# Kernel optimization log

Measured on AMD Instinct MI355X. Metric: run time of the kernel, lower is better.

The kernel has to match this reference:

```python
import math
import jax, jax.numpy as jnp
import numpy as np

N, T, F, H = 30000, 4, 128, 8  # num_node, num_type, num_fea, num_head
D = F // H


def setup_inputs() -> dict:
    key = jax.random.key(0)
    k0, k1, k2, k3, k4 = jax.random.split(key, 5)
    feature = jax.random.normal(k0, (N, F), dtype=jnp.float32)
    edge_fea = jax.random.normal(k1, (N, T, F), dtype=jnp.float32)
    node_multi_mask = jax.random.randint(k2, (N,), 0, T)
    # Xavier-uniform-like scale for [*, F, F] projection tables
    xav = math.sqrt(6.0 / (F + F))
    node_proj = jax.random.uniform(k3, (T, F, F), minval=-xav, maxval=xav, dtype=jnp.float32)
    edge_proj = jax.random.uniform(k4, (T * T, F, F), minval=-xav, maxval=xav, dtype=jnp.float32)
    return {
        "feature": feature,
        "edge_fea": edge_fea,
        "node_multi_mask": node_multi_mask,
        "node_proj": node_proj,
        "edge_proj": edge_proj,
    }


def reference(feature, edge_fea, node_multi_mask, node_proj, edge_proj):
    # Type-indexed projections. Instead of gathering per-node [F,F] matrices
    # (which would materialize N*F*F), compute projections for all T source
    # types in one batched einsum, then select each node's type with a gather.
    # node: out[n] = node_proj[mask[n]] @ feature[n]
    node_all = jnp.einsum('tgf,nf->ntg', node_proj, feature)           # [N,T,F]
    node_p = jnp.take_along_axis(node_all, node_multi_mask[:, None, None], axis=1)[:, 0]  # [N,F]
    # edge: out[n,j] = edge_proj[mask[n]*T + j] @ edge_fea[n,j]
    edge_proj_r = edge_proj.reshape(T, T, F, F)                         # [src_type, j, F, F]
    edge_all = jnp.einsum('stgf,ntf->nstg', edge_proj_r, edge_fea)      # [N,T_src,T,F]
    edge_p = jnp.take_along_axis(edge_all, node_multi_mask[:, None, None, None], axis=1)[:, 0]  # [N,T,F]

    # multi-head attention weights
    node_multi_in = node_p.reshape(N, 1, H, D).transpose(0, 2, 1, 3) / math.sqrt(D)  # [N,H,1,D]
    edge_multi_in = edge_p.reshape(N, T, H, D).transpose(0, 2, 3, 1)                  # [N,H,D,T]
    scores = jnp.matmul(node_multi_in, edge_multi_in)                                 # [N,H,1,T]
    # NOTE: original uses nn.Softmax(dim=1) -> softmax over the HEAD axis
    all_r_weight = jax.nn.softmax(scores, axis=1).transpose(0, 3, 1, 2)               # [N,T,H,1]
    return all_r_weight
```

## Files before the change

### kernel.cpp

```cpp
#include <hip/hip_runtime.h>
#include <hip/hip_bf16.h>

#define N_NODES 30000
#define T_TYPES 4
#define F_DIM   128
#define H_HEADS 8

typedef __bf16 bf16x8 __attribute__((ext_vector_type(8)));
typedef __bf16 bf16x4 __attribute__((ext_vector_type(4)));
typedef float  floatx4 __attribute__((ext_vector_type(4)));

#define WS_REORDER 64
#define WS_NPB     480256
#define WS_EPB     611328

template <int CTRL>
static __device__ __forceinline__ float dpp_add(float x) {
    int xi = __builtin_bit_cast(int, x);
    int yi = __builtin_amdgcn_update_dpp(xi, xi, CTRL, 0xF, 0xF, true);
    return x + __builtin_bit_cast(float, yi);
}
static __device__ __forceinline__ float sum16(float x) {
    x = dpp_add<0xB1>(x);
    x = dpp_add<0x4E>(x);
    x = dpp_add<0x141>(x);
    x = dpp_add<0x140>(x);
    return x;
}

__global__ __launch_bounds__(256) void prep_bucket_kernel(
    const float* __restrict__ node_proj, const float* __restrict__ edge_proj,
    const int* __restrict__ mask,
    __bf16* __restrict__ npb, __bf16* __restrict__ epb,
    int* __restrict__ counts, int* __restrict__ reorder)
{
    if (blockIdx.x < 320) {
        int i = blockIdx.x * 256 + threadIdx.x;
        int base = i * 4;
        float4 v;
        __bf16* dst;
        if (base < T_TYPES * F_DIM * F_DIM) {
            v = ((const float4*)node_proj)[i];
            dst = npb + base;
        } else {
            int off = base - T_TYPES * F_DIM * F_DIM;
            v = ((const float4*)edge_proj)[off >> 2];
            dst = epb + off;
        }
        bf16x4 w = { (__bf16)v.x, (__bf16)v.y, (__bf16)v.z, (__bf16)v.w };
        *(bf16x4*)dst = w;
    } else {
        int n = (blockIdx.x - 320) * 256 + threadIdx.x;
        int lane = threadIdx.x & 63;
        int t = (n < N_NODES) ? mask[n] : -1;
        #pragma unroll
        for (int tt = 0; tt < T_TYPES; ++tt) {
            unsigned long long bm = __ballot(t == tt);
            if (bm == 0ull) continue;
            int cnt = __popcll(bm);
            int leader = __ffsll(bm) - 1;
            int base = 0;
            if (lane == leader) base = atomicAdd(&counts[tt], cnt);
            base = __shfl(base, leader);
            if (t == tt) {
                int prefix = __popcll(bm & ((1ull << lane) - 1ull));
                reorder[tt * N_NODES + base + prefix] = n;
            }
        }
    }
}

__global__ __launch_bounds__(256, 7) void main_kernel(
    const float* __restrict__ feature, const float* __restrict__ edge_fea,
    const int* __restrict__ counts, const int* __restrict__ reorder,
    const __bf16* __restrict__ npb, const __bf16* __restrict__ epb,
    float* __restrict__ out)
{
    const int b = blockIdx.x;
    const int t = b & 3;
    const int start = (b >> 2) * 32;
    const int Nt = counts[t];
    if (start >= Nt) return;
    const int valid = min(32, Nt - start);

    __shared__ __bf16 Afeat[32][136];
    __shared__ __bf16 Aedge[32][136];
    __shared__ float  sc[32][4][H_HEADS];
    __shared__ int    nidx[32];

    const int tid = threadIdx.x;
    if (tid < 32) {
        int s = (tid < valid) ? tid : (valid - 1);
        nidx[tid] = reorder[t * N_NODES + start + s];
    }
    __syncthreads();

    const int colv = tid & 31;
    const int rowg = tid >> 5;
    #pragma unroll
    for (int it = 0; it < 4; ++it) {
        int row = it * 8 + rowg;
        float4 v = ((const float4*)(feature + (long)nidx[row] * F_DIM))[colv];
        bf16x4 w = { (__bf16)v.x, (__bf16)v.y, (__bf16)v.z, (__bf16)v.w };
        *(bf16x4*)(&Afeat[row][0] + colv * 4) = w;
    }
    __syncthreads();

    const int lane = tid & 63;
    const int wave = tid >> 6;
    const int ml   = lane & 15;
    const int quad = lane >> 4;
    const int g0   = wave * 32;

    floatx4 accN[2][2] = {};
    {
        const __bf16* a0 = &Afeat[ml][quad * 8];
        const __bf16* a1 = &Afeat[16 + ml][quad * 8];
        const __bf16* b0 = npb + t * (F_DIM * F_DIM) + (g0 + ml) * F_DIM + quad * 8;
        const __bf16* b1 = b0 + 16 * F_DIM;
        #pragma unroll
        for (int k0 = 0; k0 < 128; k0 += 32) {
            bf16x8 A0 = *(const bf16x8*)(a0 + k0);
            bf16x8 A1 = *(const bf16x8*)(a1 + k0);
            bf16x8 B0 = *(const bf16x8*)(b0 + k0);
            bf16x8 B1 = *(const bf16x8*)(b1 + k0);
            accN[0][0] = __builtin_amdgcn_mfma_f32_16x16x32_bf16(A0, B0, accN[0][0], 0, 0, 0);
            accN[0][1] = __builtin_amdgcn_mfma_f32_16x16x32_bf16(A0, B1, accN[0][1], 0, 0, 0);
            accN[1][0] = __builtin_amdgcn_mfma_f32_16x16x32_bf16(A1, B0, accN[1][0], 0, 0, 0);
            accN[1][1] = __builtin_amdgcn_mfma_f32_16x16x32_bf16(A1, B1, accN[1][1], 0, 0, 0);
        }
    }

    #pragma unroll
    for (int j = 0; j < 4; ++j) {
        if (j > 0) __syncthreads();
        #pragma unroll
        for (int it = 0; it < 4; ++it) {
            int row = it * 8 + rowg;
            float4 v = ((const float4*)(edge_fea + ((long)nidx[row] * 4 + j) * F_DIM))[colv];
            bf16x4 w = { (__bf16)v.x, (__bf16)v.y, (__bf16)v.z, (__bf16)v.w };
            *(bf16x4*)(&Aedge[row][0] + colv * 4) = w;
        }
        __syncthreads();

        floatx4 accE[2][2] = {};
        {
            const __bf16* a0 = &Aedge[ml][quad * 8];
            const __bf16* a1 = &Aedge[16 + ml][quad * 8];
            const __bf16* b0 = epb + (t * 4 + j) * (F_DIM * F_DIM) + (g0 + ml) * F_DIM + quad * 8;
            const __bf16* b1 = b0 + 16 * F_DIM;
            #pragma unroll
            for (int k0 = 0; k0 < 128; k0 += 32) {
                bf16x8 A0 = *(const bf16x8*)(a0 + k0);
                bf16x8 A1 = *(const bf16x8*)(a1 + k0);
                bf16x8 B0 = *(const bf16x8*)(b0 + k0);
                bf16x8 B1 = *(const bf16x8*)(b1 + k0);
                accE[0][0] = __builtin_amdgcn_mfma_f32_16x16x32_bf16(A0, B0, accE[0][0], 0, 0, 0);
                accE[0][1] = __builtin_amdgcn_mfma_f32_16x16x32_bf16(A0, B1, accE[0][1], 0, 0, 0);
                accE[1][0] = __builtin_amdgcn_mfma_f32_16x16x32_bf16(A1, B0, accE[1][0], 0, 0, 0);
                accE[1][1] = __builtin_amdgcn_mfma_f32_16x16x32_bf16(A1, B1, accE[1][1], 0, 0, 0);
            }
        }
        #pragma unroll
        for (int mt = 0; mt < 2; ++mt) {
            #pragma unroll
            for (int nt = 0; nt < 2; ++nt) {
                floatx4 p = accN[mt][nt] * accE[mt][nt];
                p.x = sum16(p.x);
                p.y = sum16(p.y);
                p.z = sum16(p.z);
                p.w = sum16(p.w);
                if (ml == 0) {
                    int h = wave * 2 + nt;
                    int mb = mt * 16 + quad * 4;
                    sc[mb + 0][j][h] = p.x * 0.25f;
                    sc[mb + 1][j][h] = p.y * 0.25f;
                    sc[mb + 2][j][h] = p.z * 0.25f;
                    sc[mb + 3][j][h] = p.w * 0.25f;
                }
            }
        }
    }
    __syncthreads();

    if (tid < 128) {
        int node = tid >> 2, j = tid & 3;
        if (node < valid) {
            float v[8], m = -1e30f;
            #pragma unroll
            for (int h = 0; h < 8; ++h) { v[h] = sc[node][j][h]; m = fmaxf(m, v[h]); }
            float s = 0.f;
            #pragma unroll
            for (int h = 0; h < 8; ++h) { v[h] = __expf(v[h] - m); s += v[h]; }
            float r = 1.0f / s;
            float* o = out + (long)nidx[node] * (T_TYPES * H_HEADS) + j * H_HEADS;
            float4 o0 = { v[0] * r, v[1] * r, v[2] * r, v[3] * r };
            float4 o1 = { v[4] * r, v[5] * r, v[6] * r, v[7] * r };
            ((float4*)o)[0] = o0;
            ((float4*)o)[1] = o1;
        }
    }
}

extern "C" void kernel_launch(void* const* d_in, const int* in_sizes, int n_in,
                              void* d_out, int out_size, void* d_ws, size_t ws_size,
                              hipStream_t stream) {
    const float* feature   = (const float*)d_in[0];
    const float* edge_fea  = (const float*)d_in[1];
    const int*   mask      = (const int*)d_in[2];
    const float* node_proj = (const float*)d_in[3];
    const float* edge_proj = (const float*)d_in[4];
    float* out = (float*)d_out;

    char* ws = (char*)d_ws;
    int*    counts  = (int*)ws;
    int*    reorder = (int*)(ws + WS_REORDER);
    __bf16* npb     = (__bf16*)(ws + WS_NPB);
    __bf16* epb     = (__bf16*)(ws + WS_EPB);

    hipMemsetAsync(counts, 0, 4 * sizeof(int), stream);
    prep_bucket_kernel<<<320 + (N_NODES + 255) / 256, 256, 0, stream>>>(
        node_proj, edge_proj, mask, npb, epb, counts, reorder);
    int nblk = ((N_NODES + 31) / 32) * T_TYPES;
    main_kernel<<<nblk, 256, 0, stream>>>(feature, edge_fea, counts, reorder, npb, epb, out);
}
```

Before: 146.2 us.

## Replace global type bucketing with per-block local type grouping

Drops the global atomic bucketing pass, the memset and the reorder buffer. Each block now handles 32 consecutive nodes and groups them by type locally with ballots in shared memory. All four edge rows are loaded in one pass, which removes the per-j barriers, and output writes become contiguous. In exchange, a block runs up to four partially filled 16-row MFMA tiles, one per type present, so MFMA work can roughly double. Occupancy is also lowered to 3 waves per SIMD because the shared edge buffer is larger.

```diff
diff --git a/kernel.cpp b/kernel.cpp
--- a/kernel.cpp
+++ b/kernel.cpp
@@ -5,14 +5,13 @@
 #define T_TYPES 4
 #define F_DIM   128
 #define H_HEADS 8
+#define NBLK    ((N_NODES + 31) / 32)
 
 typedef __bf16 bf16x8 __attribute__((ext_vector_type(8)));
 typedef __bf16 bf16x4 __attribute__((ext_vector_type(4)));
 typedef float  floatx4 __attribute__((ext_vector_type(4)));
 
-#define WS_REORDER 64
-#define WS_NPB     480256
-#define WS_EPB     611328
+#define WS_EPB 131072
 
 template <int CTRL>
 static __device__ __forceinline__ float dpp_add(float x) {
@@ -28,81 +27,78 @@
     return x;
 }
 
-__global__ __launch_bounds__(256) void prep_bucket_kernel(
+__global__ __launch_bounds__(256) void prep_kernel(
     const float* __restrict__ node_proj, const float* __restrict__ edge_proj,
+    __bf16* __restrict__ npb, __bf16* __restrict__ epb)
+{
+    int i = blockIdx.x * 256 + threadIdx.x;
+    int base = i * 4;
+    float4 v;
+    __bf16* dst;
+    if (base < T_TYPES * F_DIM * F_DIM) {
+        v = ((const float4*)node_proj)[i];
+        dst = npb + base;
+    } else {
+        int off = base - T_TYPES * F_DIM * F_DIM;
+        v = ((const float4*)edge_proj)[off >> 2];
+        dst = epb + off;
+    }
+    bf16x4 w = { (__bf16)v.x, (__bf16)v.y, (__bf16)v.z, (__bf16)v.w };
+    *(bf16x4*)dst = w;
+}
+
+__global__ __launch_bounds__(256, 3) void main_kernel(
+    const float* __restrict__ feature, const float* __restrict__ edge_fea,
     const int* __restrict__ mask,
-    __bf16* __restrict__ npb, __bf16* __restrict__ epb,
-    int* __restrict__ counts, int* __restrict__ reorder)
+    const __bf16* __restrict__ npb, const __bf16* __restrict__ epb,
+    float* __restrict__ out)
 {
-    if (blockIdx.x < 320) {
-        int i = blockIdx.x * 256 + threadIdx.x;
-        int base = i * 4;
-        float4 v;
-        __bf16* dst;
-        if (base < T_TYPES * F_DIM * F_DIM) {
-            v = ((const float4*)node_proj)[i];
-            dst = npb + base;
-        } else {
-            int off = base - T_TYPES * F_DIM * F_DIM;
-            v = ((const float4*)edge_proj)[off >> 2];
-            dst = epb + off;
-        }
-        bf16x4 w = { (__bf16)v.x, (__bf16)v.y, (__bf16)v.z, (__bf16)v.w };
-        *(bf16x4*)dst = w;
-    } else {
-        int n = (blockIdx.x - 320) * 256 + threadIdx.x;
-        int lane = threadIdx.x & 63;
-        int t = (n < N_NODES) ? mask[n] : -1;
+    const int n0 = blockIdx.x * 32;
+    const int valid = min(32, N_NODES - n0);
+
+    __shared__ __bf16 Afeat[32][136];
+    __shared__ __bf16 Aedge[4][32][136];
+    __shared__ float  sc[32][4][H_HEADS];
+    __shared__ int    perm[32];
+    __shared__ int    goff[T_TYPES], gcnt[T_TYPES];
+
+    const int tid = threadIdx.x;
+
+    if (tid < 64) {
+        int lane = tid;
+        int t = (lane < valid) ? mask[n0 + lane] : -1;
+        int base = 0;
         #pragma unroll
         for (int tt = 0; tt < T_TYPES; ++tt) {
             unsigned long long bm = __ballot(t == tt);
-            if (bm == 0ull) continue;
             int cnt = __popcll(bm);
-            int leader = __ffsll(bm) - 1;
-            int base = 0;
-            if (lane == leader) base = atomicAdd(&counts[tt], cnt);
-            base = __shfl(base, leader);
+            if (lane == 0) { goff[tt] = base; gcnt[tt] = cnt; }
             if (t == tt) {
-                int prefix = __popcll(bm & ((1ull << lane) - 1ull));
-                reorder[tt * N_NODES + base + prefix] = n;
+                int slot = base + __popcll(bm & ((1ull << lane) - 1ull));
+                perm[slot] = lane;
             }
+            base += cnt;
         }
     }
-}
-
-__global__ __launch_bounds__(256, 7) void main_kernel(
-    const float* __restrict__ feature, const float* __restrict__ edge_fea,
-    const int* __restrict__ counts, const int* __restrict__ reorder,
-    const __bf16* __restrict__ npb, const __bf16* __restrict__ epb,
-    float* __restrict__ out)
-{
-    const int b = blockIdx.x;
-    const int t = b & 3;
-    const int start = (b >> 2) * 32;
-    const int Nt = counts[t];
-    if (start >= Nt) return;
-    const int valid = min(32, Nt - start);
-
-    __shared__ __bf16 Afeat[32][136];
-    __shared__ __bf16 Aedge[32][136];
-    __shared__ float  sc[32][4][H_HEADS];
-    __shared__ int    nidx[32];
-
-    const int tid = threadIdx.x;
-    if (tid < 32) {
-        int s = (tid < valid) ? tid : (valid - 1);
-        nidx[tid] = reorder[t * N_NODES + start + s];
-    }
-    __syncthreads();
 
     const int colv = tid & 31;
     const int rowg = tid >> 5;
     #pragma unroll
     for (int it = 0; it < 4; ++it) {
         int row = it * 8 + rowg;
-        float4 v = ((const float4*)(feature + (long)nidx[row] * F_DIM))[colv];
+        int nl = min(row, valid - 1);
+        float4 v = ((const float4*)(feature + (long)(n0 + nl) * F_DIM))[colv];
         bf16x4 w = { (__bf16)v.x, (__bf16)v.y, (__bf16)v.z, (__bf16)v.w };
         *(bf16x4*)(&Afeat[row][0] + colv * 4) = w;
+    }
+    #pragma unroll
+    for (int it = 0; it < 16; ++it) {
+        int r = it * 8 + rowg;
+        int nl = r >> 2, j = r & 3;
+        int nc = min(nl, valid - 1);
+        float4 v = ((const float4*)(edge_fea + ((long)(n0 + nc) * 4 + j) * F_DIM))[colv];
+        bf16x4 w = { (__bf16)v.x, (__bf16)v.y, (__bf16)v.z, (__bf16)v.w };
+        *(bf16x4*)(&Aedge[j][nl][0] + colv * 4) = w;
     }
     __syncthreads();
 
@@ -112,71 +108,59 @@
     const int quad = lane >> 4;
     const int g0   = wave * 32;
 
-    floatx4 accN[2][2] = {};
-    {
-        const __bf16* a0 = &Afeat[ml][quad * 8];
-        const __bf16* a1 = &Afeat[16 + ml][quad * 8];
-        const __bf16* b0 = npb + t * (F_DIM * F_DIM) + (g0 + ml) * F_DIM + quad * 8;
-        const __bf16* b1 = b0 + 16 * F_DIM;
-        #pragma unroll
-        for (int k0 = 0; k0 < 128; k0 += 32) {
-            bf16x8 A0 = *(const bf16x8*)(a0 + k0);
-            bf16x8 A1 = *(const bf16x8*)(a1 + k0);
-            bf16x8 B0 = *(const bf16x8*)(b0 + k0);
-            bf16x8 B1 = *(const bf16x8*)(b1 + k0);
-            accN[0][0] = __builtin_amdgcn_mfma_f32_16x16x32_bf16(A0, B0, accN[0][0], 0, 0, 0);
-            accN[0][1] = __builtin_amdgcn_mfma_f32_16x16x32_bf16(A0, B1, accN[0][1], 0, 0, 0);
-            accN[1][0] = __builtin_amdgcn_mfma_f32_16x16x32_bf16(A1, B0, accN[1][0], 0, 0, 0);
-            accN[1][1] = __builtin_amdgcn_mfma_f32_16x16x32_bf16(A1, B1, accN[1][1], 0, 0, 0);
-        }
-    }
-
-    #pragma unroll
-    for (int j = 0; j < 4; ++j) {
-        if (j > 0) __syncthreads();
-        #pragma unroll
-        for (int it = 0; it < 4; ++it) {
-            int row = it * 8 + rowg;
-            float4 v = ((const float4*)(edge_fea + ((long)nidx[row] * 4 + j) * F_DIM))[colv];
-            bf16x4 w = { (__bf16)v.x, (__bf16)v.y, (__bf16)v.z, (__bf16)v.w };
-            *(bf16x4*)(&Aedge[row][0] + colv * 4) = w;
-        }
-        __syncthreads();
-
-        floatx4 accE[2][2] = {};
-        {
-            const __bf16* a0 = &Aedge[ml][quad * 8];
-            const __bf16* a1 = &Aedge[16 + ml][quad * 8];
-            const __bf16* b0 = epb + (t * 4 + j) * (F_DIM * F_DIM) + (g0 + ml) * F_DIM + quad * 8;
-            const __bf16* b1 = b0 + 16 * F_DIM;
+    for (int t = 0; t < T_TYPES; ++t) {
+        const int cnt = gcnt[t];
+        if (cnt == 0) continue;
+        const int off = goff[t];
+        for (int mi = 0; mi * 16 < cnt; ++mi) {
+            const int rA = perm[off + min(mi * 16 + ml, cnt - 1)];
+            floatx4 accN[2] = {};
+            {
+                const __bf16* aF = &Afeat[rA][quad * 8];
+                const __bf16* b0 = npb + t * (F_DIM * F_DIM) + (g0 + ml) * F_DIM + quad * 8;
+                const __bf16* b1 = b0 + 16 * F_DIM;
+                #pragma unroll
+                for (int k0 = 0; k0 < 128; k0 += 32) {
+                    bf16x8 A  = *(const bf16x8*)(aF + k0);
+                    bf16x8 B0 = *(const bf16x8*)(b0 + k0);
+                    bf16x8 B1 = *(const bf16x8*)(b1 + k0);
+                    accN[0] = __builtin_amdgcn_mfma_f32_16x16x32_bf16(A, B0, accN[0], 0, 0, 0);
+                    accN[1] = __builtin_amdgcn_mfma_f32_16x16x32_bf16(A, B1, accN[1], 0, 0, 0);
+                }
+            }
             #pragma unroll
-            for (int k0 = 0; k0 < 128; k0 += 32) {
-                bf16x8 A0 = *(const bf16x8*)(a0 + k0);
-                bf16x8 A1 = *(const bf16x8*)(a1 + k0);
-                bf16x8 B0 = *(const bf16x8*)(b0 + k0);
-                bf16x8 B1 = *(const bf16x8*)(b1 + k0);
-                accE[0][0] = __builtin_amdgcn_mfma_f32_16x16x32_bf16(A0, B0, accE[0][0], 0, 0, 0);
-                accE[0][1] = __builtin_amdgcn_mfma_f32_16x16x32_bf16(A0, B1, accE[0][1], 0, 0, 0);
-                accE[1][0] = __builtin_amdgcn_mfma_f32_16x16x32_bf16(A1, B0, accE[1][0], 0, 0, 0);
-                accE[1][1] = __builtin_amdgcn_mfma_f32_16x16x32_bf16(A1, B1, accE[1][1], 0, 0, 0);
-            }
-        }
-        #pragma unroll
-        for (int mt = 0; mt < 2; ++mt) {
-            #pragma unroll
-            for (int nt = 0; nt < 2; ++nt) {
-                floatx4 p = accN[mt][nt] * accE[mt][nt];
-                p.x = sum16(p.x);
-                p.y = sum16(p.y);
-                p.z = sum16(p.z);
-                p.w = sum16(p.w);
-                if (ml == 0) {
-                    int h = wave * 2 + nt;
-                    int mb = mt * 16 + quad * 4;
-                    sc[mb + 0][j][h] = p.x * 0.25f;
-                    sc[mb + 1][j][h] = p.y * 0.25f;
-                    sc[mb + 2][j][h] = p.z * 0.25f;
-                    sc[mb + 3][j][h] = p.w * 0.25f;
+            for (int j = 0; j < 4; ++j) {
+                floatx4 accE[2] = {};
+                {
+                    const __bf16* aE = &Aedge[j][rA][quad * 8];
+                    const __bf16* c0 = epb + (t * 4 + j) * (F_DIM * F_DIM) + (g0 + ml) * F_DIM + quad * 8;
+                    const __bf16* c1 = c0 + 16 * F_DIM;
+                    #pragma unroll
+                    for (int k0 = 0; k0 < 128; k0 += 32) {
+                        bf16x8 A  = *(const bf16x8*)(aE + k0);
+                        bf16x8 B0 = *(const bf16x8*)(c0 + k0);
+                        bf16x8 B1 = *(const bf16x8*)(c1 + k0);
+                        accE[0] = __builtin_amdgcn_mfma_f32_16x16x32_bf16(A, B0, accE[0], 0, 0, 0);
+                        accE[1] = __builtin_amdgcn_mfma_f32_16x16x32_bf16(A, B1, accE[1], 0, 0, 0);
+                    }
+                }
+                #pragma unroll
+                for (int nt = 0; nt < 2; ++nt) {
+                    floatx4 p = accN[nt] * accE[nt];
+                    p.x = sum16(p.x);
+                    p.y = sum16(p.y);
+                    p.z = sum16(p.z);
+                    p.w = sum16(p.w);
+                    if (ml == 0) {
+                        int h = wave * 2 + nt;
+                        int s0 = mi * 16 + quad * 4;
+                        float pv[4] = { p.x, p.y, p.z, p.w };
+                        #pragma unroll
+                        for (int i = 0; i < 4; ++i) {
+                            int s = s0 + i;
+                            if (s < cnt) sc[perm[off + s]][j][h] = pv[i] * 0.25f;
+                        }
+                    }
                 }
             }
         }
@@ -193,7 +177,7 @@
             #pragma unroll
             for (int h = 0; h < 8; ++h) { v[h] = __expf(v[h] - m); s += v[h]; }
             float r = 1.0f / s;
-            float* o = out + (long)nidx[node] * (T_TYPES * H_HEADS) + j * H_HEADS;
+            float* o = out + (long)(n0 + node) * (T_TYPES * H_HEADS) + j * H_HEADS;
             float4 o0 = { v[0] * r, v[1] * r, v[2] * r, v[3] * r };
             float4 o1 = { v[4] * r, v[5] * r, v[6] * r, v[7] * r };
             ((float4*)o)[0] = o0;
@@ -213,14 +197,9 @@
     float* out = (float*)d_out;
 
     char* ws = (char*)d_ws;
-    int*    counts  = (int*)ws;
-    int*    reorder = (int*)(ws + WS_REORDER);
-    __bf16* npb     = (__bf16*)(ws + WS_NPB);
-    __bf16* epb     = (__bf16*)(ws + WS_EPB);
-
-    hipMemsetAsync(counts, 0, 4 * sizeof(int), stream);
-    prep_bucket_kernel<<<320 + (N_NODES + 255) / 256, 256, 0, stream>>>(
-        node_proj, edge_proj, mask, npb, epb, counts, reorder);
-    int nblk = ((N_NODES + 31) / 32) * T_TYPES;
-    main_kernel<<<nblk, 256, 0, stream>>>(feature, edge_fea, counts, reorder, npb, epb, out);
-}
+    __bf16* npb = (__bf16*)ws;
+    __bf16* epb = (__bf16*)(ws + WS_EPB);
+
+    prep_kernel<<<320, 256, 0, stream>>>(node_proj, edge_proj, npb, epb);
+    main_kernel<<<NBLK, 256, 0, stream>>>(feature, edge_fea, mask, npb, epb, out);
+}
```

New measurement: 214.4 us. 46.7% more time.
